# Kernel tuning notes

Measured on AMD Instinct MI355X. Metric: run time of the kernel, lower is better.

The kernel has to match this reference:

```python
import jax, jax.numpy as jnp
import numpy as np

NUM_USERS = 100000
NUM_ITEMS = 100000
D = 64
B, P, N, NB, NN = 1024, 32, 64, 32, 32
W1, W2, W3 = 1.0, 0.1, 1.0


def setup_inputs() -> dict:
    key = jax.random.key(0)
    ks = jax.random.split(key, 12)
    u2e = 0.1 + 0.03 * jax.random.normal(ks[0], (NUM_USERS, D), jnp.float32)
    v2e = 0.1 + 0.03 * jax.random.normal(ks[1], (NUM_ITEMS, D), jnp.float32)
    margin_uv = jnp.ones((NUM_USERS, 1), jnp.float32)
    margin_vv = jnp.ones((NUM_ITEMS, 1), jnp.float32)
    margin_uu = jnp.ones((NUM_USERS, 1), jnp.float32)
    train_u = jax.random.randint(ks[2], (B,), 0, NUM_USERS)
    pos_idx = jax.random.randint(ks[3], (B, P), 0, NUM_ITEMS)
    neg_idx = jax.random.randint(ks[4], (B, N), 0, NUM_ITEMS)
    nb_idx = jax.random.randint(ks[5], (B, NB), 0, NUM_USERS)
    nn_idx = jax.random.randint(ks[6], (B, NN), 0, NUM_USERS)
    # ragged lengths -> padded masks
    def mk_mask(k, maxlen):
        lens = jax.random.randint(k, (B,), 1, maxlen + 1)
        return jnp.arange(maxlen)[None, :] < lens[:, None]
    pos_mask = mk_mask(ks[7], P)
    neg_mask = mk_mask(ks[8], N)
    nb_mask = mk_mask(ks[9], NB)
    nn_mask = mk_mask(ks[10], NN)
    return dict(u2e=u2e, v2e=v2e, margin_uv=margin_uv, margin_vv=margin_vv,
                margin_uu=margin_uu, train_u=train_u, pos_idx=pos_idx,
                neg_idx=neg_idx, nb_idx=nb_idx, nn_idx=nn_idx,
                pos_mask=pos_mask, neg_mask=neg_mask, nb_mask=nb_mask,
                nn_mask=nn_mask)


def reference(u2e, v2e, margin_uv, margin_vv, margin_uu, train_u, pos_idx,
              neg_idx, nb_idx, nn_idx, pos_mask, neg_mask, nb_mask, nn_mask):
    u_e = u2e[train_u]            # [B,D]
    p_e = v2e[pos_idx]            # [B,P,D]
    n_e = v2e[neg_idx]            # [B,N,D]
    nb_e = u2e[nb_idx]            # [B,NB,D]
    nn_e = u2e[nn_idx]            # [B,NN,D]
    pm = pos_mask.astype(u_e.dtype)
    nm = neg_mask.astype(u_e.dtype)
    nbm = nb_mask.astype(u_e.dtype)
    nnm = nn_mask.astype(u_e.dtype)

    # user-item triplet loss: hinge[b,i,k] = m_u[b] + ||u-p_i||^2 - ||u-n_k||^2
    d1 = jnp.sum((u_e[:, None, :] - p_e) ** 2, -1)   # [B,P]
    d2 = jnp.sum((u_e[:, None, :] - n_e) ** 2, -1)   # [B,N]
    m_u = margin_uv[train_u, 0]                       # [B]
    uv = jax.nn.relu(m_u[:, None, None] + d1[:, :, None] - d2[:, None, :])
    uv_loss = jnp.sum(uv * (pm[:, :, None] * nm[:, None, :]))

    # item-item loss (torch broadcast: margin over a separate positive axis j)
    # hinge[b,i,j,k] = m_v[b,j] + ||p_i-u||^2 - ||p_i-n_k||^2
    p2 = jnp.sum(p_e ** 2, -1)                        # [B,P]
    n2 = jnp.sum(n_e ** 2, -1)                        # [B,N]
    d2v = p2[:, :, None] + n2[:, None, :] - 2.0 * jnp.einsum('bpd,bnd->bpn', p_e, n_e)
    m_v = margin_vv[pos_idx, 0]                       # [B,P]
    hinge_vv = jax.nn.relu(m_v[:, None, :, None] + d1[:, :, None, None] - d2v[:, :, None, :])
    mask_vv = pm[:, :, None, None] * pm[:, None, :, None] * nm[:, None, None, :]
    vv_loss = jnp.sum(hinge_vv * mask_vv)

    # user-user social loss
    d1s = jnp.sum((u_e[:, None, :] - nb_e) ** 2, -1)  # [B,NB]
    d2s = jnp.sum((u_e[:, None, :] - nn_e) ** 2, -1)  # [B,NN]
    m_s = margin_uu[train_u, 0]                       # [B]
    uu = jax.nn.relu(m_s[:, None, None] + d1s[:, :, None] - d2s[:, None, :])
    uu_loss = jnp.sum(uu * (nbm[:, :, None] * nnm[:, None, :]))

    # margin regularizer (masked mean over batch positives)
    loss_am = (jnp.mean(margin_uv[train_u])
               + jnp.sum(m_v * pm) / jnp.sum(pm)
               + jnp.mean(margin_uu[train_u]))

    return uv_loss + W1 * vv_loss + W3 * uu_loss + W2 * loss_am
```

## Files before the change

### kernel.cpp

```cpp
#include <hip/hip_runtime.h>
#include <cfloat>

#define BB   1024
#define PP   32
#define NNEG 64
#define DD   64
#define BSTR 72
#define SSTR 66

static constexpr float W2c = 0.1f;

typedef __attribute__((ext_vector_type(8)))  short bf16x8;
typedef __attribute__((ext_vector_type(16))) float f32x16;

__device__ __forceinline__ short f2bf(float f) {
    unsigned u = __float_as_uint(f);
    unsigned r = (u + 0x7fffu + ((u >> 16) & 1u)) >> 16;
    return (short)r;
}

__device__ __forceinline__ float parse_mask(const void* p, int flag, int j) {
    if (flag == 1) return ((const unsigned char*)p)[j] ? 1.0f : 0.0f;
    if (flag == 2) return (((const float*)p)[j] != 0.0f) ? 1.0f : 0.0f;
    return ((const int*)p)[j] ? 1.0f : 0.0f;
}

__global__ __launch_bounds__(256) void loss_kernel(
    const float* __restrict__ u2e, const float* __restrict__ v2e,
    const float* __restrict__ margin_uv, const float* __restrict__ margin_vv,
    const float* __restrict__ margin_uu,
    const int* __restrict__ train_u, const int* __restrict__ pos_idx,
    const int* __restrict__ neg_idx, const int* __restrict__ nb_idx,
    const int* __restrict__ nn_idx,
    const void* __restrict__ pos_mask, const void* __restrict__ neg_mask,
    const void* __restrict__ nb_mask, const void* __restrict__ nn_mask,
    float* __restrict__ ws) {

    const int b = blockIdx.x;
    const int t = threadIdx.x;
    const int lane = t & 63;
    const int w = t >> 6;

    __shared__ __align__(16) short pn_bf[96 * BSTR];
    __shared__ __align__(16) float s_lds[PP * SSTR];
    __shared__ __align__(16) float u_s[DD];
    __shared__ float d1[PP], p2s[PP], d2[NNEG], n2s[NNEG], d1sA[PP], d2sA[PP];
    __shared__ float pmf[PP], nmf[NNEG], nbmf[PP], nnmf[PP];
    __shared__ float mvp[PP], mv_arr[PP], s_srt[PP], S_suf[PP + 1];
    __shared__ int   pos_i[PP], neg_i[NNEG], nb_i[PP], nn_i[PP];
    __shared__ float sc[2];
    __shared__ float red[4][3];
    __shared__ int   wflags[4][2];

    const int tu = train_u[b];

    {
        unsigned int mw = ((const unsigned int*)pos_mask)[t];
        int f32hit  = (mw == 0x3f800000u) ? 1 : 0;
        int bytehit = (!f32hit && (mw & 0xFFFFFF00u)) ? 1 : 0;
        int wf = __any(f32hit) ? 1 : 0;
        int wb = __any(bytehit) ? 1 : 0;
        if (lane == 0) { wflags[w][0] = wf; wflags[w][1] = wb; }
    }
    if (t < DD) u_s[t] = u2e[(size_t)tu * DD + t];
    if (t < PP)              pos_i[t]       = pos_idx[b * PP + t];
    else if (t < 96)         neg_i[t - PP]  = neg_idx[b * NNEG + (t - PP)];
    else if (t < 128)        nb_i[t - 96]   = nb_idx[b * PP + (t - 96)];
    else if (t < 160)        nn_i[t - 128]  = nn_idx[b * PP + (t - 128)];
    if (t == 0) { sc[0] = margin_uv[tu]; sc[1] = margin_uu[tu]; }
    __syncthreads();

    const int flag = (wflags[0][0] | wflags[1][0] | wflags[2][0] | wflags[3][0]) ? 2
                   : ((wflags[0][1] | wflags[1][1] | wflags[2][1] | wflags[3][1]) ? 1 : 0);

    float4 ch[6]; int dstRow[6], dstQ[6];
    #pragma unroll
    for (int r = 0; r < 6; ++r) {
        int c = t + 256 * r;
        int row = c >> 4, q = c & 15;
        int gidx = (row < PP) ? pos_i[row] : neg_i[row - PP];
        ch[r]   = *(const float4*)(v2e + (size_t)gidx * DD + 4 * q);
        dstRow[r] = row; dstQ[r] = q;
    }
    if (t < PP) {
        float pm = parse_mask(pos_mask, flag, b * PP + t);
        float mv = margin_vv[pos_i[t]];
        pmf[t] = pm; mv_arr[t] = mv;
        mvp[t] = (pm != 0.0f) ? mv : -FLT_MAX;
    } else if (t < 96) {
        nmf[t - PP] = parse_mask(neg_mask, flag, b * NNEG + (t - PP));
    } else if (t < 128) {
        nbmf[t - 96] = parse_mask(nb_mask, flag, b * PP + (t - 96));
    } else if (t < 160) {
        nnmf[t - 128] = parse_mask(nn_mask, flag, b * PP + (t - 128));
    }
    {
        int row = t >> 2, q4 = t & 3;
        int idx = (row < PP) ? nb_i[row] : nn_i[row - PP];
        const float* rp = u2e + (size_t)idx * DD + 16 * q4;
        float s = 0.0f;
        #pragma unroll
        for (int q = 0; q < 4; ++q) {
            float4 e  = *(const float4*)(rp + 4 * q);
            float4 uu = *(const float4*)(u_s + 16 * q4 + 4 * q);
            float dx = e.x - uu.x, dy = e.y - uu.y, dz = e.z - uu.z, dw = e.w - uu.w;
            s += dx * dx + dy * dy + dz * dz + dw * dw;
        }
        s += __shfl_xor(s, 1);
        s += __shfl_xor(s, 2);
        if (q4 == 0) { if (row < PP) d1sA[row] = s; else d2sA[row - PP] = s; }
    }
    #pragma unroll
    for (int r = 0; r < 6; ++r) {
        short4 s4 = make_short4(f2bf(ch[r].x), f2bf(ch[r].y), f2bf(ch[r].z), f2bf(ch[r].w));
        *(short4*)(pn_bf + dstRow[r] * BSTR + 4 * dstQ[r]) = s4;
    }
    __syncthreads();

    if (w < 2) {
        f32x16 acc;
        #pragma unroll
        for (int i = 0; i < 16; ++i) acc[i] = 0.0f;
        const int lr = lane & 31;
        const int hi = lane >> 5;
        const short* ap = pn_bf + lr * BSTR;
        const short* bp = pn_bf + (PP + 32 * w + lr) * BSTR;
        #pragma unroll
        for (int c = 0; c < 4; ++c) {
            const int d0 = 16 * c + 8 * hi;
            bf16x8 a = *(const bf16x8*)(ap + d0);
            bf16x8 bfr = *(const bf16x8*)(bp + d0);
            acc = __builtin_amdgcn_mfma_f32_32x32x16_bf16(a, bfr, acc, 0, 0, 0);
        }
        #pragma unroll
        for (int r = 0; r < 16; ++r) {
            const int m = (r & 3) + 8 * (r >> 2) + 4 * hi;
            s_lds[m * SSTR + 32 * w + lr] = acc[r];
        }
    } else if (w == 2) {
        const int k = lane;
        const float* rp = v2e + (size_t)neg_i[k] * DD;
        float sd = 0.0f, sq = 0.0f;
        #pragma unroll
        for (int q = 0; q < 16; ++q) {
            float4 e  = *(const float4*)(rp + 4 * q);
            float4 uu = *(const float4*)(u_s + 4 * q);
            float dx = e.x - uu.x, dy = e.y - uu.y, dz = e.z - uu.z, dw = e.w - uu.w;
            sd += dx * dx + dy * dy + dz * dz + dw * dw;
            sq += e.x * e.x + e.y * e.y + e.z * e.z + e.w * e.w;
        }
        d2[k] = sd; n2s[k] = sq;
    } else {
        if (lane < PP) {
            const float* rp = v2e + (size_t)pos_i[lane] * DD;
            float sd = 0.0f, sq = 0.0f;
            #pragma unroll
            for (int q = 0; q < 16; ++q) {
                float4 e  = *(const float4*)(rp + 4 * q);
                float4 uu = *(const float4*)(u_s + 4 * q);
                float dx = e.x - uu.x, dy = e.y - uu.y, dz = e.z - uu.z, dw = e.w - uu.w;
                sd += dx * dx + dy * dy + dz * dz + dw * dw;
                sq += e.x * e.x + e.y * e.y + e.z * e.z + e.w * e.w;
            }
            d1[lane] = sd; p2s[lane] = sq;
        } else {
            const int l2 = lane - PP;
            float vj = mvp[l2];
            int r = 0;
            #pragma unroll
            for (int j = 0; j < PP; ++j) {
                float o = mvp[j];
                r += (o < vj || (o == vj && j < l2)) ? 1 : 0;
            }
            s_srt[r] = vj;
            __threadfence_block();
            float y = s_srt[l2];
            #pragma unroll
            for (int d = 1; d < PP; d <<= 1) {
                float z = __shfl_down(y, d);
                if (l2 + d < PP) y += z;
            }
            S_suf[l2] = y;
            if (l2 == 0) S_suf[PP] = 0.0f;
        }
    }
    __syncthreads();

    const float m_u = sc[0], m_s = sc[1];
    const float s31 = s_srt[PP - 1];
    const int kb = t & 15;
    const int ib = t >> 4;
    float loss = 0.0f;
    #pragma unroll
    for (int a = 0; a < 2; ++a) {
        const int i = ib + 16 * a;
        const float d1i = d1[i], p2i = p2s[i], pmi = pmf[i];
        #pragma unroll
        for (int c = 0; c < 4; ++c) {
            const int k = kb + 16 * c;
            const float Sik = s_lds[i * SSTR + k];
            const float cc = d1i - (p2i + n2s[k] - 2.0f * Sik);
            const float v = -cc;
            int t0 = 0;
            #pragma unroll
            for (int st = 16; st > 0; st >>= 1)
                t0 += (s_srt[t0 + st - 1] <= v) ? st : 0;
            t0 += (s31 <= v) ? 1 : 0;
            const float inner = S_suf[t0] + (float)(PP - t0) * cc;
            const float uvh = fmaxf(m_u + d1i - d2[k], 0.0f);
            loss += pmi * nmf[k] * (inner + uvh);
        }
    }

    #pragma unroll
    for (int rr = 0; rr < 4; ++rr) {
        int pid = t + 256 * rr;
        int i = pid >> 5, k = pid & 31;
        loss += nbmf[i] * nnmf[k] * fmaxf(m_s + d1sA[i] - d2sA[k], 0.0f);
    }

    float a2 = (t < PP) ? mv_arr[t] * pmf[t] : 0.0f;
    float a3 = (t < PP) ? pmf[t] : 0.0f;
    #pragma unroll
    for (int m = 1; m < 64; m <<= 1) {
        loss += __shfl_xor(loss, m);
        a2   += __shfl_xor(a2, m);
        a3   += __shfl_xor(a3, m);
    }
    if (lane == 0) { red[w][0] = loss; red[w][1] = a2; red[w][2] = a3; }
    __syncthreads();
    if (t == 0) {
        float S0 = 0, S2 = 0, S3 = 0;
        for (int i = 0; i < 4; ++i) { S0 += red[i][0]; S2 += red[i][1]; S3 += red[i][2]; }
        ws[0 * BB + b] = S0;
        ws[1 * BB + b] = sc[0];
        ws[2 * BB + b] = S2;
        ws[3 * BB + b] = S3;
        ws[4 * BB + b] = sc[1];
    }
}

__global__ __launch_bounds__(256) void finalize_kernel(const float* __restrict__ ws,
                                                       float* __restrict__ out) {
    __shared__ float red[4][5];
    const int t = threadIdx.x, lane = t & 63, w = t >> 6;
    float s[5] = {0, 0, 0, 0, 0};
    for (int i = t; i < BB; i += 256)
        #pragma unroll
        for (int a = 0; a < 5; ++a) s[a] += ws[a * BB + i];
    #pragma unroll
    for (int m = 1; m < 64; m <<= 1)
        #pragma unroll
        for (int a = 0; a < 5; ++a) s[a] += __shfl_xor(s[a], m);
    if (lane == 0)
        #pragma unroll
        for (int a = 0; a < 5; ++a) red[w][a] = s[a];
    __syncthreads();
    if (t == 0) {
        float S[5];
        #pragma unroll
        for (int a = 0; a < 5; ++a) {
            S[a] = 0;
            for (int i = 0; i < 4; ++i) S[a] += red[i][a];
        }
        float loss_am = S[1] / (float)BB + S[2] / S[3] + S[4] / (float)BB;
        out[0] = S[0] + W2c * loss_am;
    }
}

extern "C" void kernel_launch(void* const* d_in, const int* in_sizes, int n_in,
                              void* d_out, int out_size, void* d_ws, size_t ws_size,
                              hipStream_t stream) {
    const float* u2e       = (const float*)d_in[0];
    const float* v2e       = (const float*)d_in[1];
    const float* margin_uv = (const float*)d_in[2];
    const float* margin_vv = (const float*)d_in[3];
    const float* margin_uu = (const float*)d_in[4];
    const int*   train_u   = (const int*)d_in[5];
    const int*   pos_idx   = (const int*)d_in[6];
    const int*   neg_idx   = (const int*)d_in[7];
    const int*   nb_idx    = (const int*)d_in[8];
    const int*   nn_idx    = (const int*)d_in[9];
    const void*  pos_mask  = d_in[10];
    const void*  neg_mask  = d_in[11];
    const void*  nb_mask   = d_in[12];
    const void*  nn_mask   = d_in[13];

    float* ws  = (float*)d_ws;
    float* out = (float*)d_out;

    loss_kernel<<<BB, 256, 0, stream>>>(u2e, v2e, margin_uv, margin_vv, margin_uu,
                                        train_u, pos_idx, neg_idx, nb_idx, nn_idx,
                                        pos_mask, neg_mask, nb_mask, nn_mask, ws);
    finalize_kernel<<<1, 256, 0, stream>>>(ws, out);
}
```

Measured before the change: 21.50 us.

## Double block size and fuse row norms into the shared gather

The loss kernel now launches 512 threads per block instead of 256. Each thread gathers its share of the pos/neg rows once and computes the partial distance and squared-norm terms in registers, reducing them with shuffles. This replaces the separate warps that re-read every v2e row from global memory after the gather. The social-distance and loss loops are respread over the larger block. The trade-off is more threads per block and tighter launch bounds, which may limit registers or occupancy.

```diff
diff --git a/kernel.cpp b/kernel.cpp
--- a/kernel.cpp
+++ b/kernel.cpp
@@ -25,7 +25,7 @@
     return ((const int*)p)[j] ? 1.0f : 0.0f;
 }
 
-__global__ __launch_bounds__(256) void loss_kernel(
+__global__ __launch_bounds__(512, 8) void loss_kernel(
     const float* __restrict__ u2e, const float* __restrict__ v2e,
     const float* __restrict__ margin_uv, const float* __restrict__ margin_vv,
     const float* __restrict__ margin_uu,
@@ -49,8 +49,8 @@
     __shared__ float mvp[PP], mv_arr[PP], s_srt[PP], S_suf[PP + 1];
     __shared__ int   pos_i[PP], neg_i[NNEG], nb_i[PP], nn_i[PP];
     __shared__ float sc[2];
-    __shared__ float red[4][3];
-    __shared__ int   wflags[4][2];
+    __shared__ float red[8][3];
+    __shared__ int   wflags[8][2];
 
     const int tu = train_u[b];
 
@@ -70,17 +70,42 @@
     if (t == 0) { sc[0] = margin_uv[tu]; sc[1] = margin_uu[tu]; }
     __syncthreads();
 
-    const int flag = (wflags[0][0] | wflags[1][0] | wflags[2][0] | wflags[3][0]) ? 2
-                   : ((wflags[0][1] | wflags[1][1] | wflags[2][1] | wflags[3][1]) ? 1 : 0);
-
-    float4 ch[6]; int dstRow[6], dstQ[6];
-    #pragma unroll
-    for (int r = 0; r < 6; ++r) {
-        int c = t + 256 * r;
-        int row = c >> 4, q = c & 15;
-        int gidx = (row < PP) ? pos_i[row] : neg_i[row - PP];
-        ch[r]   = *(const float4*)(v2e + (size_t)gidx * DD + 4 * q);
-        dstRow[r] = row; dstQ[r] = q;
+    const int flag = (wflags[0][0] | wflags[1][0] | wflags[2][0] | wflags[3][0] |
+                      wflags[4][0] | wflags[5][0] | wflags[6][0] | wflags[7][0]) ? 2
+                   : ((wflags[0][1] | wflags[1][1] | wflags[2][1] | wflags[3][1] |
+                       wflags[4][1] | wflags[5][1] | wflags[6][1] | wflags[7][1]) ? 1 : 0);
+
+    const int q  = t & 15;
+    const int R0 = t >> 4;
+    const float4 u4 = *(const float4*)(u_s + 4 * q);
+    float4 ch[3];
+    float sdp[3], sqp[3];
+    #pragma unroll
+    for (int r = 0; r < 3; ++r) {
+        const int R = R0 + 32 * r;
+        const int gidx = (R < PP) ? pos_i[R] : neg_i[R - PP];
+        ch[r] = *(const float4*)(v2e + (size_t)gidx * DD + 4 * q);
+        float dx = ch[r].x - u4.x, dy = ch[r].y - u4.y,
+              dz = ch[r].z - u4.z, dw = ch[r].w - u4.w;
+        sdp[r] = dx * dx + dy * dy + dz * dz + dw * dw;
+        sqp[r] = ch[r].x * ch[r].x + ch[r].y * ch[r].y
+               + ch[r].z * ch[r].z + ch[r].w * ch[r].w;
+    }
+    #pragma unroll
+    for (int m = 1; m < 16; m <<= 1) {
+        #pragma unroll
+        for (int r = 0; r < 3; ++r) {
+            sdp[r] += __shfl_xor(sdp[r], m);
+            sqp[r] += __shfl_xor(sqp[r], m);
+        }
+    }
+    if (q == 0) {
+        #pragma unroll
+        for (int r = 0; r < 3; ++r) {
+            const int R = R0 + 32 * r;
+            if (R < PP) { d1[R] = sdp[r]; p2s[R] = sqp[r]; }
+            else        { d2[R - PP] = sdp[r]; n2s[R - PP] = sqp[r]; }
+        }
     }
     if (t < PP) {
         float pm = parse_mask(pos_mask, flag, b * PP + t);
@@ -95,25 +120,27 @@
         nnmf[t - 128] = parse_mask(nn_mask, flag, b * PP + (t - 128));
     }
     {
-        int row = t >> 2, q4 = t & 3;
-        int idx = (row < PP) ? nb_i[row] : nn_i[row - PP];
-        const float* rp = u2e + (size_t)idx * DD + 16 * q4;
-        float s = 0.0f;
-        #pragma unroll
-        for (int q = 0; q < 4; ++q) {
-            float4 e  = *(const float4*)(rp + 4 * q);
-            float4 uu = *(const float4*)(u_s + 16 * q4 + 4 * q);
-            float dx = e.x - uu.x, dy = e.y - uu.y, dz = e.z - uu.z, dw = e.w - uu.w;
-            s += dx * dx + dy * dy + dz * dz + dw * dw;
-        }
+        const int row = t >> 3, sub = t & 7;
+        const int idx = (row < PP) ? nb_i[row] : nn_i[row - PP];
+        const float* rp = u2e + (size_t)idx * DD + 8 * sub;
+        float4 e0 = *(const float4*)(rp);
+        float4 e1 = *(const float4*)(rp + 4);
+        float4 v0 = *(const float4*)(u_s + 8 * sub);
+        float4 v1 = *(const float4*)(u_s + 8 * sub + 4);
+        float dx = e0.x - v0.x, dy = e0.y - v0.y, dz = e0.z - v0.z, dw = e0.w - v0.w;
+        float s = dx * dx + dy * dy + dz * dz + dw * dw;
+        dx = e1.x - v1.x; dy = e1.y - v1.y; dz = e1.z - v1.z; dw = e1.w - v1.w;
+        s += dx * dx + dy * dy + dz * dz + dw * dw;
         s += __shfl_xor(s, 1);
         s += __shfl_xor(s, 2);
-        if (q4 == 0) { if (row < PP) d1sA[row] = s; else d2sA[row - PP] = s; }
-    }
-    #pragma unroll
-    for (int r = 0; r < 6; ++r) {
+        s += __shfl_xor(s, 4);
+        if (sub == 0) { if (row < PP) d1sA[row] = s; else d2sA[row - PP] = s; }
+    }
+    #pragma unroll
+    for (int r = 0; r < 3; ++r) {
+        const int R = R0 + 32 * r;
         short4 s4 = make_short4(f2bf(ch[r].x), f2bf(ch[r].y), f2bf(ch[r].z), f2bf(ch[r].w));
-        *(short4*)(pn_bf + dstRow[r] * BSTR + 4 * dstQ[r]) = s4;
+        *(short4*)(pn_bf + R * BSTR + 4 * q) = s4;
     }
     __syncthreads();
 
@@ -128,7 +155,7 @@
         #pragma unroll
         for (int c = 0; c < 4; ++c) {
             const int d0 = 16 * c + 8 * hi;
-            bf16x8 a = *(const bf16x8*)(ap + d0);
+            bf16x8 a   = *(const bf16x8*)(ap + d0);
             bf16x8 bfr = *(const bf16x8*)(bp + d0);
             acc = __builtin_amdgcn_mfma_f32_32x32x16_bf16(a, bfr, acc, 0, 0, 0);
         }
@@ -137,86 +164,54 @@
             const int m = (r & 3) + 8 * (r >> 2) + 4 * hi;
             s_lds[m * SSTR + 32 * w + lr] = acc[r];
         }
-    } else if (w == 2) {
-        const int k = lane;
-        const float* rp = v2e + (size_t)neg_i[k] * DD;
-        float sd = 0.0f, sq = 0.0f;
-        #pragma unroll
-        for (int q = 0; q < 16; ++q) {
-            float4 e  = *(const float4*)(rp + 4 * q);
-            float4 uu = *(const float4*)(u_s + 4 * q);
-            float dx = e.x - uu.x, dy = e.y - uu.y, dz = e.z - uu.z, dw = e.w - uu.w;
-            sd += dx * dx + dy * dy + dz * dz + dw * dw;
-            sq += e.x * e.x + e.y * e.y + e.z * e.z + e.w * e.w;
-        }
-        d2[k] = sd; n2s[k] = sq;
-    } else {
-        if (lane < PP) {
-            const float* rp = v2e + (size_t)pos_i[lane] * DD;
-            float sd = 0.0f, sq = 0.0f;
-            #pragma unroll
-            for (int q = 0; q < 16; ++q) {
-                float4 e  = *(const float4*)(rp + 4 * q);
-                float4 uu = *(const float4*)(u_s + 4 * q);
-                float dx = e.x - uu.x, dy = e.y - uu.y, dz = e.z - uu.z, dw = e.w - uu.w;
-                sd += dx * dx + dy * dy + dz * dz + dw * dw;
-                sq += e.x * e.x + e.y * e.y + e.z * e.z + e.w * e.w;
-            }
-            d1[lane] = sd; p2s[lane] = sq;
-        } else {
-            const int l2 = lane - PP;
-            float vj = mvp[l2];
-            int r = 0;
-            #pragma unroll
-            for (int j = 0; j < PP; ++j) {
-                float o = mvp[j];
-                r += (o < vj || (o == vj && j < l2)) ? 1 : 0;
-            }
-            s_srt[r] = vj;
-            __threadfence_block();
-            float y = s_srt[l2];
-            #pragma unroll
-            for (int d = 1; d < PP; d <<= 1) {
-                float z = __shfl_down(y, d);
-                if (l2 + d < PP) y += z;
-            }
-            S_suf[l2] = y;
-            if (l2 == 0) S_suf[PP] = 0.0f;
-        }
+    } else if (w == 2 && lane < PP) {
+        float vj = mvp[lane];
+        int r = 0;
+        #pragma unroll
+        for (int j = 0; j < PP; ++j) {
+            float o = mvp[j];
+            r += (o < vj || (o == vj && j < lane)) ? 1 : 0;
+        }
+        s_srt[r] = vj;
+        __threadfence_block();
+        float y = s_srt[lane];
+        #pragma unroll
+        for (int d = 1; d < PP; d <<= 1) {
+            float z = __shfl_down(y, d);
+            if (lane + d < PP) y += z;
+        }
+        S_suf[lane] = y;
+        if (lane == 0) S_suf[PP] = 0.0f;
     }
     __syncthreads();
 
     const float m_u = sc[0], m_s = sc[1];
     const float s31 = s_srt[PP - 1];
     const int kb = t & 15;
-    const int ib = t >> 4;
+    const int i  = t >> 4;
+    const float d1i = d1[i], p2i = p2s[i], pmi = pmf[i];
     float loss = 0.0f;
     #pragma unroll
-    for (int a = 0; a < 2; ++a) {
-        const int i = ib + 16 * a;
-        const float d1i = d1[i], p2i = p2s[i], pmi = pmf[i];
-        #pragma unroll
-        for (int c = 0; c < 4; ++c) {
-            const int k = kb + 16 * c;
-            const float Sik = s_lds[i * SSTR + k];
-            const float cc = d1i - (p2i + n2s[k] - 2.0f * Sik);
-            const float v = -cc;
-            int t0 = 0;
-            #pragma unroll
-            for (int st = 16; st > 0; st >>= 1)
-                t0 += (s_srt[t0 + st - 1] <= v) ? st : 0;
-            t0 += (s31 <= v) ? 1 : 0;
-            const float inner = S_suf[t0] + (float)(PP - t0) * cc;
-            const float uvh = fmaxf(m_u + d1i - d2[k], 0.0f);
-            loss += pmi * nmf[k] * (inner + uvh);
-        }
-    }
-
-    #pragma unroll
-    for (int rr = 0; rr < 4; ++rr) {
-        int pid = t + 256 * rr;
-        int i = pid >> 5, k = pid & 31;
-        loss += nbmf[i] * nnmf[k] * fmaxf(m_s + d1sA[i] - d2sA[k], 0.0f);
+    for (int c = 0; c < 4; ++c) {
+        const int k = kb + 16 * c;
+        const float Sik = s_lds[i * SSTR + k];
+        const float cc = d1i - (p2i + n2s[k] - 2.0f * Sik);
+        const float v = -cc;
+        int t0 = 0;
+        #pragma unroll
+        for (int st = 16; st > 0; st >>= 1)
+            t0 += (s_srt[t0 + st - 1] <= v) ? st : 0;
+        t0 += (s31 <= v) ? 1 : 0;
+        const float inner = S_suf[t0] + (float)(PP - t0) * cc;
+        const float uvh = fmaxf(m_u + d1i - d2[k], 0.0f);
+        loss += pmi * nmf[k] * (inner + uvh);
+    }
+
+    #pragma unroll
+    for (int rr = 0; rr < 2; ++rr) {
+        int pid = t + 512 * rr;
+        int ii = pid >> 5, k = pid & 31;
+        loss += nbmf[ii] * nnmf[k] * fmaxf(m_s + d1sA[ii] - d2sA[k], 0.0f);
     }
 
     float a2 = (t < PP) ? mv_arr[t] * pmf[t] : 0.0f;
@@ -231,7 +226,8 @@
     __syncthreads();
     if (t == 0) {
         float S0 = 0, S2 = 0, S3 = 0;
-        for (int i = 0; i < 4; ++i) { S0 += red[i][0]; S2 += red[i][1]; S3 += red[i][2]; }
+        #pragma unroll
+        for (int i2 = 0; i2 < 8; ++i2) { S0 += red[i2][0]; S2 += red[i2][1]; S3 += red[i2][2]; }
         ws[0 * BB + b] = S0;
         ws[1 * BB + b] = sc[0];
         ws[2 * BB + b] = S2;
@@ -289,7 +285,7 @@
     float* ws  = (float*)d_ws;
     float* out = (float*)d_out;
 
-    loss_kernel<<<BB, 256, 0, stream>>>(u2e, v2e, margin_uv, margin_vv, margin_uu,
+    loss_kernel<<<BB, 512, 0, stream>>>(u2e, v2e, margin_uv, margin_vv, margin_uu,
                                         train_u, pos_idx, neg_idx, nb_idx, nn_idx,
                                         pos_mask, neg_mask, nb_mask, nn_mask, ws);
     finalize_kernel<<<1, 256, 0, stream>>>(ws, out);
```

Result: no change. 21.37 us (-0.6%).
